# Kernel tuning notes

Hardware: AMD Instinct MI355X
Metric: run time of the kernel (lower is better)

Reference implementation:

```python
import jax, jax.numpy as jnp
import numpy as np

HID = 256
N_HEADS = 4
ATTN_DIM = HID // N_HEADS  # 64
B, S = 64, 512
NEG = -1e10


def setup_inputs() -> dict:
    key = jax.random.key(0)
    ks = jax.random.split(key, 12)
    def lin(k, fan_in, shape):
        bound = 1.0 / np.sqrt(fan_in)
        return jax.random.uniform(k, shape, jnp.float32, -bound, bound)
    return {
        "query": jax.random.normal(ks[0], (B, S, HID), jnp.float32),
        "key": jax.random.normal(ks[1], (B, S, HID), jnp.float32),
        "value": jax.random.normal(ks[2], (B, S, HID), jnp.float32),
        "mask": jax.random.randint(ks[3], (B, 1, S, S), 0, 2, jnp.int32),
        "Wq": lin(ks[4], HID, (HID, HID)), "bq": lin(ks[5], HID, (HID,)),
        "Wk": lin(ks[6], HID, (HID, HID)), "bk": lin(ks[7], HID, (HID,)),
        "Wv": lin(ks[8], HID, (HID, ATTN_DIM)), "bv": lin(ks[9], HID, (ATTN_DIM,)),
        "Wh": lin(ks[10], ATTN_DIM, (ATTN_DIM, HID)), "bh": lin(ks[11], ATTN_DIM, (HID,)),
    }


def reference(query, key, value, mask, Wq, bq, Wk, bk, Wv, bv, Wh, bh):
    b = query.shape[0]
    scale = jnp.sqrt(jnp.asarray(ATTN_DIM, query.dtype))
    Q = (query @ Wq + bq).reshape(b, -1, N_HEADS, ATTN_DIM).transpose(0, 2, 1, 3)  # [B,H,Sq,d]
    K = (key @ Wk + bk).reshape(b, -1, N_HEADS, ATTN_DIM).transpose(0, 2, 1, 3)    # [B,H,Sk,d]
    V = value @ Wv + bv                                                            # [B,Sk,d]
    energy = jnp.einsum('bhqd,bhkd->bhqk', Q, K) / scale
    energy = jnp.where(mask == 0, jnp.asarray(NEG, energy.dtype), energy)
    probs = jax.nn.softmax(energy, axis=-1)          # [B,H,Sq,Sk]
    attention = jnp.mean(probs, axis=1)              # head-mean, [B,Sq,Sk]
    # dropout is identity in eval mode
    output = jnp.einsum('bqk,bkd->bqd', attention, V) @ Wh + bh  # [B,Sq,HID]
    return output, attention
```

## Files before the change

kernel.cpp:

```cpp
#include <hip/hip_runtime.h>

#define NB 64
#define SS 512
#define HIDD 256
#define NHEADS 4
#define ADIM 64
#define NTOT 576

typedef __attribute__((ext_vector_type(8))) short short8v;
typedef __attribute__((ext_vector_type(4))) float f32x4;

#define MFMA16(A, B, C) __builtin_amdgcn_mfma_f32_16x16x32_bf16(A, B, C, 0, 0, 0)
#define AS1 __attribute__((address_space(1)))
#define AS3 __attribute__((address_space(3)))

__device__ __forceinline__ void g2l16(void* lds, const void* g) {
    __builtin_amdgcn_global_load_lds((const AS1 unsigned*)g,
                                     (AS3 unsigned*)lds, 16, 0, 0);
}

__device__ __forceinline__ void bsplit(float x, short& hi, short& lo) {
    unsigned u = __float_as_uint(x);
    unsigned uh = (u + 0x8000u) & 0xFFFF0000u;
    hi = (short)(uh >> 16);
    float r = x - __uint_as_float(uh);
    lo = (short)((__float_as_uint(r) + 0x8000u) >> 16);
}

__device__ __forceinline__ void bsplit_v(float x, short8v& vh, short8v& vl, int i) {
    short h, l;
    bsplit(x, h, l);
    vh[i] = h;
    vl[i] = l;
}

__device__ __forceinline__ short bf16r(float x) {
    return (short)((__float_as_uint(x) + 0x8000u) >> 16);
}

__device__ __forceinline__ int frag_addr(int bb, int hh, int s, int d) {
    const int t16 = s >> 4, rk = s & 15;
    const int ks2 = d >> 5, lgk = (d >> 3) & 3, e8 = d & 7;
    return ((((bb * 4 + hh) * 32 + t16) * 2 + ks2) * 64 + rk + 16 * lgk) * 8 + e8;
}

__global__ __launch_bounds__(256) void prep_weights(
    const float* __restrict__ Wq, const float* __restrict__ Wk,
    const float* __restrict__ Wv, const float* __restrict__ Wh,
    short* __restrict__ WT_hi, short* __restrict__ WT_lo,
    short* __restrict__ WhT)
{
    const int bx = blockIdx.x;
    if (bx < NTOT) {
        const int idx = bx * 256 + threadIdx.x;
        const int n = idx >> 8, k = idx & 255;
        float v;
        if (n < 256)      v = Wq[k * 256 + n];
        else if (n < 512) v = Wk[k * 256 + (n - 256)];
        else              v = Wv[k * 64 + (n - 512)];
        short h, l;
        bsplit(v, h, l);
        WT_hi[idx] = h;
        WT_lo[idx] = l;
    } else {
        const int idx2 = (bx - NTOT) * 256 + threadIdx.x;
        const int n = idx2 >> 6, d = idx2 & 63;
        WhT[idx2] = bf16r(Wh[d * HIDD + n]);
    }
}

__global__ __launch_bounds__(256) void qkv_qk(
    const float* __restrict__ query, const float* __restrict__ key,
    const short* __restrict__ WT_hi, const short* __restrict__ WT_lo,
    const float* __restrict__ bq, const float* __restrict__ bk,
    short* __restrict__ Qhi, short* __restrict__ Qlo,
    short* __restrict__ Khi, short* __restrict__ Klo)
{
    __shared__ short Ws_h[2][256 * 32];
    __shared__ short Ws_l[2][256 * 32];

    const int bm = blockIdx.x * 64;
    const int y = blockIdx.y;
    const int nrow0 = y << 8;
    const float* A = y ? key : query;
    const float* biasp = y ? bk : bq;
    short* Dhi = y ? Khi : Qhi;
    short* Dlo = y ? Klo : Qlo;

    const int tid = threadIdx.x;
    const int w = tid >> 6, l = tid & 63;
    const int l15 = l & 15, lg = l >> 4;
    const int wbase = tid & 192;

    auto stageWT = [&](int buf, int kc) {
#pragma unroll
        for (int i = 0; i < 4; ++i) {
            const int g = i * 256 + tid;
            const int row = g >> 2;
            const int p = g & 3;
            const int sl = p ^ (row & 3);
            const size_t goff = (size_t)(nrow0 + row) * HIDD + kc * 32 + sl * 8;
            g2l16(&Ws_h[buf][(i * 256 + wbase) * 8], WT_hi + goff);
            g2l16(&Ws_l[buf][(i * 256 + wbase) * 8], WT_lo + goff);
        }
    };

    const float* arow = A + (size_t)(bm + w * 16 + l15) * HIDD + lg * 8;

    f32x4 acc[16];
#pragma unroll
    for (int jn = 0; jn < 16; ++jn) acc[jn] = (f32x4){0.f, 0.f, 0.f, 0.f};

    float4 a0c = *reinterpret_cast<const float4*>(arow);
    float4 a1c = *reinterpret_cast<const float4*>(arow + 4);
    stageWT(0, 0);
    __syncthreads();

    int cur = 0;
#pragma unroll
    for (int kc = 0; kc < 8; ++kc) {
        float4 a0n, a1n;
        if (kc < 7) {
            a0n = *reinterpret_cast<const float4*>(arow + (kc + 1) * 32);
            a1n = *reinterpret_cast<const float4*>(arow + (kc + 1) * 32 + 4);
            stageWT(cur ^ 1, kc + 1);
        }

        short8v ah, al;
        bsplit_v(a0c.x, ah, al, 0);
        bsplit_v(a0c.y, ah, al, 1);
        bsplit_v(a0c.z, ah, al, 2);
        bsplit_v(a0c.w, ah, al, 3);
        bsplit_v(a1c.x, ah, al, 4);
        bsplit_v(a1c.y, ah, al, 5);
        bsplit_v(a1c.z, ah, al, 6);
        bsplit_v(a1c.w, ah, al, 7);

#pragma unroll
        for (int jn = 0; jn < 16; ++jn) {
            const int rowB = jn * 16 + l15;
            const int c = lg ^ (rowB & 3);
            short8v bh = *reinterpret_cast<const short8v*>(&Ws_h[cur][rowB * 32 + c * 8]);
            short8v bl = *reinterpret_cast<const short8v*>(&Ws_l[cur][rowB * 32 + c * 8]);
            acc[jn] = MFMA16(ah, bh, acc[jn]);
            acc[jn] = MFMA16(ah, bl, acc[jn]);
            acc[jn] = MFMA16(al, bh, acc[jn]);
        }
        __syncthreads();
        cur ^= 1;
        if (kc < 7) { a0c = a0n; a1c = a1n; }
    }

#pragma unroll
    for (int jn = 0; jn < 16; ++jn) {
        const int ncol = jn * 16 + l15;
        const float bias = biasp[ncol];
        const int hh = ncol >> 6, dd = ncol & 63;
#pragma unroll
        for (int r = 0; r < 4; ++r) {
            const int m = bm + w * 16 + lg * 4 + r;
            const int bb = m >> 9, s = m & 511;
            const int fa = frag_addr(bb, hh, s, dd);
            short h, lo_;
            bsplit(acc[jn][r] + bias, h, lo_);
            Dhi[fa] = h;
            Dlo[fa] = lo_;
        }
    }
}

__global__ __launch_bounds__(256) void qkv_v(
    const float* __restrict__ value,
    const short* __restrict__ WT_hi, const short* __restrict__ WT_lo,
    const float* __restrict__ bv, short* __restrict__ VT)
{
    __shared__ short Ws_h[2][64 * 32];
    __shared__ short Ws_l[2][64 * 32];

    const int bm = blockIdx.x * 64;
    const int tid = threadIdx.x;
    const int w = tid >> 6, l = tid & 63;
    const int l15 = l & 15, lg = l >> 4;
    const int wbase = tid & 192;

    auto stageWT = [&](int buf, int kc) {
        const int row = tid >> 2;
        const int p = tid & 3;
        const int sl = p ^ (row & 3);
        const size_t goff = (size_t)(512 + row) * HIDD + kc * 32 + sl * 8;
        g2l16(&Ws_h[buf][wbase * 8], WT_hi + goff);
        g2l16(&Ws_l[buf][wbase * 8], WT_lo + goff);
    };

    const float* arow = value + (size_t)(bm + w * 16 + l15) * HIDD + lg * 8;

    f32x4 acc[4];
#pragma unroll
    for (int jn = 0; jn < 4; ++jn) acc[jn] = (f32x4){0.f, 0.f, 0.f, 0.f};

    float4 a0c = *reinterpret_cast<const float4*>(arow);
    float4 a1c = *reinterpret_cast<const float4*>(arow + 4);
    stageWT(0, 0);
    __syncthreads();

    int cur = 0;
#pragma unroll
    for (int kc = 0; kc < 8; ++kc) {
        float4 a0n, a1n;
        if (kc < 7) {
            a0n = *reinterpret_cast<const float4*>(arow + (kc + 1) * 32);
            a1n = *reinterpret_cast<const float4*>(arow + (kc + 1) * 32 + 4);
            stageWT(cur ^ 1, kc + 1);
        }

        short8v ah, al;
        bsplit_v(a0c.x, ah, al, 0);
        bsplit_v(a0c.y, ah, al, 1);
        bsplit_v(a0c.z, ah, al, 2);
        bsplit_v(a0c.w, ah, al, 3);
        bsplit_v(a1c.x, ah, al, 4);
        bsplit_v(a1c.y, ah, al, 5);
        bsplit_v(a1c.z, ah, al, 6);
        bsplit_v(a1c.w, ah, al, 7);

#pragma unroll
        for (int jn = 0; jn < 4; ++jn) {
            const int rowB = jn * 16 + l15;
            const int c = lg ^ (rowB & 3);
            short8v bh = *reinterpret_cast<const short8v*>(&Ws_h[cur][rowB * 32 + c * 8]);
            short8v bl = *reinterpret_cast<const short8v*>(&Ws_l[cur][rowB * 32 + c * 8]);
            acc[jn] = MFMA16(ah, bh, acc[jn]);
            acc[jn] = MFMA16(ah, bl, acc[jn]);
            acc[jn] = MFMA16(al, bh, acc[jn]);
        }
        __syncthreads();
        cur ^= 1;
        if (kc < 7) { a0c = a0n; a1c = a1n; }
    }

#pragma unroll
    for (int jn = 0; jn < 4; ++jn) {
        const int d = jn * 16 + l15;
        const float bias = bv[d];
#pragma unroll
        for (int r = 0; r < 4; ++r) {
            const int m = bm + w * 16 + lg * 4 + r;
            const int bb = m >> 9, kk = m & 511;
            const int ks = kk >> 5;
            const int lane = l15 + 16 * ((kk >> 3) & 3);
            const int idx = (((bb * 4 + jn) * 16 + ks) * 64 + lane) * 8 + (kk & 7);
            VT[idx] = bf16r(acc[jn][r] + bias);
        }
    }
}

__global__ __launch_bounds__(256) void attn_probs_fused(
    const short* __restrict__ Qhi_g, const short* __restrict__ Qlo_g,
    const short* __restrict__ Khi_g, const short* __restrict__ Klo_g,
    const short* __restrict__ VT, const short* __restrict__ WhT,
    const int* __restrict__ mask, const float* __restrict__ bh,
    float* __restrict__ attn, float* __restrict__ out)
{
    __shared__ __align__(16) short P_s[32 * 512];
    __shared__ float red[2][4][2][16];

    const int wg = blockIdx.x;
    const int swz = (wg & 7) * 128 + (wg >> 3);
    const int b = swz >> 4;
    const int q0 = (swz & 15) * 32;

    const int tid = threadIdx.x;
    const int w = tid >> 6;
    const int l = tid & 63;
    const int l15 = l & 15;
    const int lg = l >> 4;

    unsigned mbits[2];
#pragma unroll
    for (int qs = 0; qs < 2; ++qs) {
        unsigned bits = 0;
        const int q = q0 + qs * 16 + l15;
        const int* mrow = mask + ((size_t)b * SS + q) * SS;
#pragma unroll
        for (int f = 0; f < 8; ++f) {
            const int kt = f >> 1, ms = f & 1;
            const int k = kt * 128 + (2 * w + ms) * 16 + lg * 4;
            int4 mv = *reinterpret_cast<const int4*>(&mrow[k]);
            bits |= (mv.x != 0 ? 1u : 0u) << (f * 4 + 0);
            bits |= (mv.y != 0 ? 1u : 0u) << (f * 4 + 1);
            bits |= (mv.z != 0 ? 1u : 0u) << (f * 4 + 2);
            bits |= (mv.w != 0 ? 1u : 0u) << (f * 4 + 3);
        }
        mbits[qs] = bits;
    }

    f32x4 acc[4][2][2];
#pragma unroll
    for (int kt = 0; kt < 4; ++kt)
#pragma unroll
        for (int ms = 0; ms < 2; ++ms)
#pragma unroll
            for (int qs = 0; qs < 2; ++qs)
                acc[kt][ms][qs] = (f32x4){0.f, 0.f, 0.f, 0.f};

    const int qt_base = (swz & 15) * 2;

    for (int h = 0; h < NHEADS; ++h) {
        const int bh32 = (b * 4 + h) * 32;

        short8v qh[2][2], ql[2][2];
#pragma unroll
        for (int ks2 = 0; ks2 < 2; ++ks2)
#pragma unroll
            for (int qs = 0; qs < 2; ++qs) {
                const int off = (((bh32 + qt_base + qs) * 2 + ks2) * 64 + l) * 8;
                qh[ks2][qs] = *reinterpret_cast<const short8v*>(Qhi_g + off);
                ql[ks2][qs] = *reinterpret_cast<const short8v*>(Qlo_g + off);
            }

        f32x4 e[4][2][2];
#pragma unroll
        for (int kt = 0; kt < 4; ++kt)
#pragma unroll
            for (int ms = 0; ms < 2; ++ms)
#pragma unroll
                for (int qs = 0; qs < 2; ++qs)
                    e[kt][ms][qs] = (f32x4){0.f, 0.f, 0.f, 0.f};

#pragma unroll
        for (int kt = 0; kt < 4; ++kt) {
#pragma unroll
            for (int ks2 = 0; ks2 < 2; ++ks2) {
                const int t0 = kt * 8 + 2 * w;
                const int base0 = (((bh32 + t0) * 2 + ks2) * 64 + l) * 8;
                const int base1 = base0 + 1024;
                short8v ah0 = *reinterpret_cast<const short8v*>(Khi_g + base0);
                short8v ah1 = *reinterpret_cast<const short8v*>(Khi_g + base1);
                short8v al0 = *reinterpret_cast<const short8v*>(Klo_g + base0);
                short8v al1 = *reinterpret_cast<const short8v*>(Klo_g + base1);

                e[kt][0][0] = MFMA16(ah0, qh[ks2][0], e[kt][0][0]);
                e[kt][0][0] = MFMA16(ah0, ql[ks2][0], e[kt][0][0]);
                e[kt][0][0] = MFMA16(al0, qh[ks2][0], e[kt][0][0]);

                e[kt][0][1] = MFMA16(ah0, qh[ks2][1], e[kt][0][1]);
                e[kt][0][1] = MFMA16(ah0, ql[ks2][1], e[kt][0][1]);
                e[kt][0][1] = MFMA16(al0, qh[ks2][1], e[kt][0][1]);

                e[kt][1][0] = MFMA16(ah1, qh[ks2][0], e[kt][1][0]);
                e[kt][1][0] = MFMA16(ah1, ql[ks2][0], e[kt][1][0]);
                e[kt][1][0] = MFMA16(al1, qh[ks2][0], e[kt][1][0]);

                e[kt][1][1] = MFMA16(ah1, qh[ks2][1], e[kt][1][1]);
                e[kt][1][1] = MFMA16(ah1, ql[ks2][1], e[kt][1][1]);
                e[kt][1][1] = MFMA16(al1, qh[ks2][1], e[kt][1][1]);
            }
        }

        float sm[2] = {0.f, 0.f};
        const float c = 0.125f;
#pragma unroll
        for (int kt = 0; kt < 4; ++kt)
#pragma unroll
            for (int ms = 0; ms < 2; ++ms)
#pragma unroll
                for (int qs = 0; qs < 2; ++qs)
#pragma unroll
                    for (int r = 0; r < 4; ++r) {
                        float p = __expf(e[kt][ms][qs][r] * c);
                        const unsigned bit = (mbits[qs] >> ((kt * 2 + ms) * 4 + r)) & 1u;
                        p = bit ? p : 0.f;
                        e[kt][ms][qs][r] = p;
                        sm[qs] += p;
                    }
#pragma unroll
        for (int qs = 0; qs < 2; ++qs) {
            sm[qs] += __shfl_xor(sm[qs], 16);
            sm[qs] += __shfl_xor(sm[qs], 32);
        }
        if (l < 16) { red[h & 1][w][0][l] = sm[0]; red[h & 1][w][1][l] = sm[1]; }
        __syncthreads();
#pragma unroll
        for (int qs = 0; qs < 2; ++qs) {
            const float Z = (red[h & 1][0][qs][l15] + red[h & 1][1][qs][l15]) +
                            (red[h & 1][2][qs][l15] + red[h & 1][3][qs][l15]);
            const float inv = 0.25f / fmaxf(Z, 1e-30f);
#pragma unroll
            for (int kt = 0; kt < 4; ++kt)
#pragma unroll
                for (int ms = 0; ms < 2; ++ms)
#pragma unroll
                    for (int r = 0; r < 4; ++r)
                        acc[kt][ms][qs][r] += e[kt][ms][qs][r] * inv;
        }
    }

#pragma unroll
    for (int kt = 0; kt < 4; ++kt)
#pragma unroll
        for (int ms = 0; ms < 2; ++ms)
#pragma unroll
            for (int qs = 0; qs < 2; ++qs) {
                const int q = q0 + qs * 16 + l15;
                const int k = kt * 128 + (2 * w + ms) * 16 + lg * 4;
                float4 o;
                o.x = acc[kt][ms][qs][0];
                o.y = acc[kt][ms][qs][1];
                o.z = acc[kt][ms][qs][2];
                o.w = acc[kt][ms][qs][3];
                *reinterpret_cast<float4*>(&attn[((size_t)b * SS + q) * SS + k]) = o;

                const int ql_ = qs * 16 + l15;
                const int c8 = kt * 16 + (2 * w + ms) * 2 + (lg >> 1);
                const int phys = c8 ^ (ql_ & 7);
                short4 pk;
                pk.x = bf16r(acc[kt][ms][qs][0]);
                pk.y = bf16r(acc[kt][ms][qs][1]);
                pk.z = bf16r(acc[kt][ms][qs][2]);
                pk.w = bf16r(acc[kt][ms][qs][3]);
                *reinterpret_cast<short4*>(&P_s[ql_ * 512 + phys * 8 + (lg & 1) * 4]) = pk;
            }
    __syncthreads();

    f32x4 tacc[2];
    tacc[0] = (f32x4){0.f, 0.f, 0.f, 0.f};
    tacc[1] = (f32x4){0.f, 0.f, 0.f, 0.f};
#pragma unroll
    for (int ks = 0; ks < 16; ++ks) {
        short8v va = *reinterpret_cast<const short8v*>(
            VT + (((b * 4 + w) * 16 + ks) * 64 + l) * 8);
#pragma unroll
        for (int qt = 0; qt < 2; ++qt) {
            const int q = qt * 16 + l15;
            const int phys = (ks * 4 + lg) ^ (q & 7);
            short8v pb = *reinterpret_cast<const short8v*>(&P_s[q * 512 + phys * 8]);
            tacc[qt] = MFMA16(va, pb, tacc[qt]);
        }
    }
    __syncthreads();

    float* T_s = reinterpret_cast<float*>(P_s);
#pragma unroll
    for (int qt = 0; qt < 2; ++qt) {
        const int q = qt * 16 + l15;
        const int d = w * 16 + lg * 4;
        float4 tv;
        tv.x = tacc[qt][0];
        tv.y = tacc[qt][1];
        tv.z = tacc[qt][2];
        tv.w = tacc[qt][3];
        *reinterpret_cast<float4*>(&T_s[q * 68 + d]) = tv;
    }
    __syncthreads();

    f32x4 oacc[2][4];
#pragma unroll
    for (int qt = 0; qt < 2; ++qt)
#pragma unroll
        for (int nt = 0; nt < 4; ++nt)
            oacc[qt][nt] = (f32x4){0.f, 0.f, 0.f, 0.f};

#pragma unroll
    for (int ks = 0; ks < 2; ++ks) {
        short8v ta[2];
#pragma unroll
        for (int qt = 0; qt < 2; ++qt) {
            const int q = qt * 16 + l15;
            float4 t0 = *reinterpret_cast<const float4*>(&T_s[q * 68 + ks * 32 + lg * 8]);
            float4 t1 = *reinterpret_cast<const float4*>(&T_s[q * 68 + ks * 32 + lg * 8 + 4]);
            ta[qt][0] = bf16r(t0.x);
            ta[qt][1] = bf16r(t0.y);
            ta[qt][2] = bf16r(t0.z);
            ta[qt][3] = bf16r(t0.w);
            ta[qt][4] = bf16r(t1.x);
            ta[qt][5] = bf16r(t1.y);
            ta[qt][6] = bf16r(t1.z);
            ta[qt][7] = bf16r(t1.w);
        }
#pragma unroll
        for (int nt = 0; nt < 4; ++nt) {
            const int n = (w * 4 + nt) * 16 + l15;
            short8v wb = *reinterpret_cast<const short8v*>(
                WhT + n * 64 + ks * 32 + lg * 8);
#pragma unroll
            for (int qt = 0; qt < 2; ++qt)
                oacc[qt][nt] = MFMA16(ta[qt], wb, oacc[qt][nt]);
        }
    }

#pragma unroll
    for (int qt = 0; qt < 2; ++qt)
#pragma unroll
        for (int nt = 0; nt < 4; ++nt) {
            const int n = (w * 4 + nt) * 16 + l15;
            const float bias = bh[n];
#pragma unroll
            for (int r = 0; r < 4; ++r) {
                const int q = q0 + qt * 16 + lg * 4 + r;
                out[((size_t)b * SS + q) * HIDD + n] = oacc[qt][nt][r] + bias;
            }
        }
}

extern "C" void kernel_launch(void* const* d_in, const int* in_sizes, int n_in,
                              void* d_out, int out_size, void* d_ws, size_t ws_size,
                              hipStream_t stream)
{
    const float* query = (const float*)d_in[0];
    const float* key   = (const float*)d_in[1];
    const float* value = (const float*)d_in[2];
    const int*   mask  = (const int*)d_in[3];
    const float* Wq = (const float*)d_in[4];
    const float* bq = (const float*)d_in[5];
    const float* Wk = (const float*)d_in[6];
    const float* bk = (const float*)d_in[7];
    const float* Wv = (const float*)d_in[8];
    const float* bv = (const float*)d_in[9];
    const float* Wh = (const float*)d_in[10];
    const float* bh = (const float*)d_in[11];

    float* out  = (float*)d_out;
    float* attn = out + (size_t)NB * SS * HIDD;

    const size_t BS = (size_t)NB * SS;
    short* Qhi = (short*)d_ws;
    short* Qlo = Qhi + BS * HIDD;
    short* Khi = Qlo + BS * HIDD;
    short* Klo = Khi + BS * HIDD;
    short* VT  = Klo + BS * HIDD;
    short* WhT = VT + BS * ADIM;

    short* WT_hi = (short*)attn;
    short* WT_lo = WT_hi + NTOT * HIDD;

    prep_weights<<<dim3(NTOT + 64), 256, 0, stream>>>(Wq, Wk, Wv, Wh,
                                                      WT_hi, WT_lo, WhT);
    qkv_qk<<<dim3(512, 2), 256, 0, stream>>>(query, key, WT_hi, WT_lo,
                                             bq, bk, Qhi, Qlo, Khi, Klo);
    qkv_v<<<dim3(512), 256, 0, stream>>>(value, WT_hi, WT_lo, bv, VT);
    attn_probs_fused<<<dim3(1024), 256, 0, stream>>>(Qhi, Qlo, Khi, Klo, VT, WhT,
                                                     mask, bh, attn, out);
}
```

Baseline: 154.8 us.

## Drop bf16 hi/lo split for Q/K and double attention waves per block

Q and K are now stored as single bf16 values, with no hi/lo pair. This halves their workspace writes and reads and cuts the QK^T MFMAs from three per tile to one. The attention kernel now launches 512 threads, so 8 waves split the key dimension where 4 did before, and the softmax-sum reduction covers 8 partials. Only the first 4 waves run the P·V and output projection stages. The risk is lower precision in the attention probabilities, since a single bf16 product replaces the split-precision emulation.

After: 138.8 us. 10.3% less time.

```diff
diff --git a/kernel.cpp b/kernel.cpp
--- a/kernel.cpp
+++ b/kernel.cpp
@@ -73,8 +73,7 @@
     const float* __restrict__ query, const float* __restrict__ key,
     const short* __restrict__ WT_hi, const short* __restrict__ WT_lo,
     const float* __restrict__ bq, const float* __restrict__ bk,
-    short* __restrict__ Qhi, short* __restrict__ Qlo,
-    short* __restrict__ Khi, short* __restrict__ Klo)
+    short* __restrict__ Qhi, short* __restrict__ Khi)
 {
     __shared__ short Ws_h[2][256 * 32];
     __shared__ short Ws_l[2][256 * 32];
@@ -85,7 +84,6 @@
     const float* A = y ? key : query;
     const float* biasp = y ? bk : bq;
     short* Dhi = y ? Khi : Qhi;
-    short* Dlo = y ? Klo : Qlo;
 
     const int tid = threadIdx.x;
     const int w = tid >> 6, l = tid & 63;
@@ -161,10 +159,7 @@
             const int m = bm + w * 16 + lg * 4 + r;
             const int bb = m >> 9, s = m & 511;
             const int fa = frag_addr(bb, hh, s, dd);
-            short h, lo_;
-            bsplit(acc[jn][r] + bias, h, lo_);
-            Dhi[fa] = h;
-            Dlo[fa] = lo_;
+            Dhi[fa] = bf16r(acc[jn][r] + bias);
         }
     }
 }
@@ -254,15 +249,14 @@
     }
 }
 
-__global__ __launch_bounds__(256) void attn_probs_fused(
-    const short* __restrict__ Qhi_g, const short* __restrict__ Qlo_g,
-    const short* __restrict__ Khi_g, const short* __restrict__ Klo_g,
+__global__ __launch_bounds__(512) void attn_probs_fused(
+    const short* __restrict__ Qhi_g, const short* __restrict__ Khi_g,
     const short* __restrict__ VT, const short* __restrict__ WhT,
     const int* __restrict__ mask, const float* __restrict__ bh,
     float* __restrict__ attn, float* __restrict__ out)
 {
     __shared__ __align__(16) short P_s[32 * 512];
-    __shared__ float red[2][4][2][16];
+    __shared__ float red[2][8][2][16];
 
     const int wg = blockIdx.x;
     const int swz = (wg & 7) * 128 + (wg >> 3);
@@ -271,6 +265,8 @@
 
     const int tid = threadIdx.x;
     const int w = tid >> 6;
+    const int h2 = w >> 2;
+    const int sp = w & 3;
     const int l = tid & 63;
     const int l15 = l & 15;
     const int lg = l >> 4;
@@ -282,95 +278,84 @@
         const int q = q0 + qs * 16 + l15;
         const int* mrow = mask + ((size_t)b * SS + q) * SS;
 #pragma unroll
-        for (int f = 0; f < 8; ++f) {
-            const int kt = f >> 1, ms = f & 1;
-            const int k = kt * 128 + (2 * w + ms) * 16 + lg * 4;
-            int4 mv = *reinterpret_cast<const int4*>(&mrow[k]);
-            bits |= (mv.x != 0 ? 1u : 0u) << (f * 4 + 0);
-            bits |= (mv.y != 0 ? 1u : 0u) << (f * 4 + 1);
-            bits |= (mv.z != 0 ? 1u : 0u) << (f * 4 + 2);
-            bits |= (mv.w != 0 ? 1u : 0u) << (f * 4 + 3);
-        }
+        for (int kl = 0; kl < 2; ++kl)
+#pragma unroll
+            for (int ms = 0; ms < 2; ++ms) {
+                const int fi = kl * 2 + ms;
+                const int kt = 2 * h2 + kl;
+                const int k = kt * 128 + (2 * sp + ms) * 16 + lg * 4;
+                int4 mv = *reinterpret_cast<const int4*>(&mrow[k]);
+                bits |= (mv.x != 0 ? 1u : 0u) << (fi * 4 + 0);
+                bits |= (mv.y != 0 ? 1u : 0u) << (fi * 4 + 1);
+                bits |= (mv.z != 0 ? 1u : 0u) << (fi * 4 + 2);
+                bits |= (mv.w != 0 ? 1u : 0u) << (fi * 4 + 3);
+            }
         mbits[qs] = bits;
     }
 
-    f32x4 acc[4][2][2];
-#pragma unroll
-    for (int kt = 0; kt < 4; ++kt)
+    f32x4 acc[2][2][2];
+#pragma unroll
+    for (int kl = 0; kl < 2; ++kl)
 #pragma unroll
         for (int ms = 0; ms < 2; ++ms)
 #pragma unroll
             for (int qs = 0; qs < 2; ++qs)
-                acc[kt][ms][qs] = (f32x4){0.f, 0.f, 0.f, 0.f};
+                acc[kl][ms][qs] = (f32x4){0.f, 0.f, 0.f, 0.f};
 
     const int qt_base = (swz & 15) * 2;
 
     for (int h = 0; h < NHEADS; ++h) {
         const int bh32 = (b * 4 + h) * 32;
 
-        short8v qh[2][2], ql[2][2];
+        short8v qh[2][2];
 #pragma unroll
         for (int ks2 = 0; ks2 < 2; ++ks2)
 #pragma unroll
             for (int qs = 0; qs < 2; ++qs) {
                 const int off = (((bh32 + qt_base + qs) * 2 + ks2) * 64 + l) * 8;
                 qh[ks2][qs] = *reinterpret_cast<const short8v*>(Qhi_g + off);
-                ql[ks2][qs] = *reinterpret_cast<const short8v*>(Qlo_g + off);
-            }
-
-        f32x4 e[4][2][2];
-#pragma unroll
-        for (int kt = 0; kt < 4; ++kt)
+            }
+
+        f32x4 e[2][2][2];
+#pragma unroll
+        for (int kl = 0; kl < 2; ++kl)
 #pragma unroll
             for (int ms = 0; ms < 2; ++ms)
 #pragma unroll
                 for (int qs = 0; qs < 2; ++qs)
-                    e[kt][ms][qs] = (f32x4){0.f, 0.f, 0.f, 0.f};
-
-#pragma unroll
-        for (int kt = 0; kt < 4; ++kt) {
+                    e[kl][ms][qs] = (f32x4){0.f, 0.f, 0.f, 0.f};
+
+#pragma unroll
+        for (int kl = 0; kl < 2; ++kl) {
+            const int t0 = (2 * h2 + kl) * 8 + 2 * sp;
 #pragma unroll
             for (int ks2 = 0; ks2 < 2; ++ks2) {
-                const int t0 = kt * 8 + 2 * w;
                 const int base0 = (((bh32 + t0) * 2 + ks2) * 64 + l) * 8;
                 const int base1 = base0 + 1024;
                 short8v ah0 = *reinterpret_cast<const short8v*>(Khi_g + base0);
                 short8v ah1 = *reinterpret_cast<const short8v*>(Khi_g + base1);
-                short8v al0 = *reinterpret_cast<const short8v*>(Klo_g + base0);
-                short8v al1 = *reinterpret_cast<const short8v*>(Klo_g + base1);
-
-                e[kt][0][0] = MFMA16(ah0, qh[ks2][0], e[kt][0][0]);
-                e[kt][0][0] = MFMA16(ah0, ql[ks2][0], e[kt][0][0]);
-                e[kt][0][0] = MFMA16(al0, qh[ks2][0], e[kt][0][0]);
-
-                e[kt][0][1] = MFMA16(ah0, qh[ks2][1], e[kt][0][1]);
-                e[kt][0][1] = MFMA16(ah0, ql[ks2][1], e[kt][0][1]);
-                e[kt][0][1] = MFMA16(al0, qh[ks2][1], e[kt][0][1]);
-
-                e[kt][1][0] = MFMA16(ah1, qh[ks2][0], e[kt][1][0]);
-                e[kt][1][0] = MFMA16(ah1, ql[ks2][0], e[kt][1][0]);
-                e[kt][1][0] = MFMA16(al1, qh[ks2][0], e[kt][1][0]);
-
-                e[kt][1][1] = MFMA16(ah1, qh[ks2][1], e[kt][1][1]);
-                e[kt][1][1] = MFMA16(ah1, ql[ks2][1], e[kt][1][1]);
-                e[kt][1][1] = MFMA16(al1, qh[ks2][1], e[kt][1][1]);
+
+                e[kl][0][0] = MFMA16(ah0, qh[ks2][0], e[kl][0][0]);
+                e[kl][0][1] = MFMA16(ah0, qh[ks2][1], e[kl][0][1]);
+                e[kl][1][0] = MFMA16(ah1, qh[ks2][0], e[kl][1][0]);
+                e[kl][1][1] = MFMA16(ah1, qh[ks2][1], e[kl][1][1]);
             }
         }
 
         float sm[2] = {0.f, 0.f};
         const float c = 0.125f;
 #pragma unroll
-        for (int kt = 0; kt < 4; ++kt)
+        for (int kl = 0; kl < 2; ++kl)
 #pragma unroll
             for (int ms = 0; ms < 2; ++ms)
 #pragma unroll
                 for (int qs = 0; qs < 2; ++qs)
 #pragma unroll
                     for (int r = 0; r < 4; ++r) {
-                        float p = __expf(e[kt][ms][qs][r] * c);
-                        const unsigned bit = (mbits[qs] >> ((kt * 2 + ms) * 4 + r)) & 1u;
+                        float p = __expf(e[kl][ms][qs][r] * c);
+                        const unsigned bit = (mbits[qs] >> ((kl * 2 + ms) * 4 + r)) & 1u;
                         p = bit ? p : 0.f;
-                        e[kt][ms][qs][r] = p;
+                        e[kl][ms][qs][r] = p;
                         sm[qs] += p;
                     }
 #pragma unroll
@@ -382,42 +367,44 @@
         __syncthreads();
 #pragma unroll
         for (int qs = 0; qs < 2; ++qs) {
-            const float Z = (red[h & 1][0][qs][l15] + red[h & 1][1][qs][l15]) +
-                            (red[h & 1][2][qs][l15] + red[h & 1][3][qs][l15]);
+            float Z = 0.f;
+#pragma unroll
+            for (int wv = 0; wv < 8; ++wv) Z += red[h & 1][wv][qs][l15];
             const float inv = 0.25f / fmaxf(Z, 1e-30f);
 #pragma unroll
-            for (int kt = 0; kt < 4; ++kt)
+            for (int kl = 0; kl < 2; ++kl)
 #pragma unroll
                 for (int ms = 0; ms < 2; ++ms)
 #pragma unroll
                     for (int r = 0; r < 4; ++r)
-                        acc[kt][ms][qs][r] += e[kt][ms][qs][r] * inv;
-        }
-    }
-
-#pragma unroll
-    for (int kt = 0; kt < 4; ++kt)
+                        acc[kl][ms][qs][r] += e[kl][ms][qs][r] * inv;
+        }
+    }
+
+#pragma unroll
+    for (int kl = 0; kl < 2; ++kl)
 #pragma unroll
         for (int ms = 0; ms < 2; ++ms)
 #pragma unroll
             for (int qs = 0; qs < 2; ++qs) {
+                const int kt = 2 * h2 + kl;
                 const int q = q0 + qs * 16 + l15;
-                const int k = kt * 128 + (2 * w + ms) * 16 + lg * 4;
+                const int k = kt * 128 + (2 * sp + ms) * 16 + lg * 4;
                 float4 o;
-                o.x = acc[kt][ms][qs][0];
-                o.y = acc[kt][ms][qs][1];
-                o.z = acc[kt][ms][qs][2];
-                o.w = acc[kt][ms][qs][3];
+                o.x = acc[kl][ms][qs][0];
+                o.y = acc[kl][ms][qs][1];
+                o.z = acc[kl][ms][qs][2];
+                o.w = acc[kl][ms][qs][3];
                 *reinterpret_cast<float4*>(&attn[((size_t)b * SS + q) * SS + k]) = o;
 
                 const int ql_ = qs * 16 + l15;
-                const int c8 = kt * 16 + (2 * w + ms) * 2 + (lg >> 1);
+                const int c8 = kt * 16 + (2 * sp + ms) * 2 + (lg >> 1);
                 const int phys = c8 ^ (ql_ & 7);
                 short4 pk;
-                pk.x = bf16r(acc[kt][ms][qs][0]);
-                pk.y = bf16r(acc[kt][ms][qs][1]);
-                pk.z = bf16r(acc[kt][ms][qs][2]);
-                pk.w = bf16r(acc[kt][ms][qs][3]);
+                pk.x = bf16r(acc[kl][ms][qs][0]);
+                pk.y = bf16r(acc[kl][ms][qs][1]);
+                pk.z = bf16r(acc[kl][ms][qs][2]);
+                pk.w = bf16r(acc[kl][ms][qs][3]);
                 *reinterpret_cast<short4*>(&P_s[ql_ * 512 + phys * 8 + (lg & 1) * 4]) = pk;
             }
     __syncthreads();
@@ -425,81 +412,87 @@
     f32x4 tacc[2];
     tacc[0] = (f32x4){0.f, 0.f, 0.f, 0.f};
     tacc[1] = (f32x4){0.f, 0.f, 0.f, 0.f};
-#pragma unroll
-    for (int ks = 0; ks < 16; ++ks) {
-        short8v va = *reinterpret_cast<const short8v*>(
-            VT + (((b * 4 + w) * 16 + ks) * 64 + l) * 8);
+    if (w < 4) {
+#pragma unroll
+        for (int ks = 0; ks < 16; ++ks) {
+            short8v va = *reinterpret_cast<const short8v*>(
+                VT + (((b * 4 + w) * 16 + ks) * 64 + l) * 8);
+#pragma unroll
+            for (int qt = 0; qt < 2; ++qt) {
+                const int q = qt * 16 + l15;
+                const int phys = (ks * 4 + lg) ^ (q & 7);
+                short8v pb = *reinterpret_cast<const short8v*>(&P_s[q * 512 + phys * 8]);
+                tacc[qt] = MFMA16(va, pb, tacc[qt]);
+            }
+        }
+    }
+    __syncthreads();
+
+    float* T_s = reinterpret_cast<float*>(P_s);
+    if (w < 4) {
 #pragma unroll
         for (int qt = 0; qt < 2; ++qt) {
             const int q = qt * 16 + l15;
-            const int phys = (ks * 4 + lg) ^ (q & 7);
-            short8v pb = *reinterpret_cast<const short8v*>(&P_s[q * 512 + phys * 8]);
-            tacc[qt] = MFMA16(va, pb, tacc[qt]);
+            const int d = w * 16 + lg * 4;
+            float4 tv;
+            tv.x = tacc[qt][0];
+            tv.y = tacc[qt][1];
+            tv.z = tacc[qt][2];
+            tv.w = tacc[qt][3];
+            *reinterpret_cast<float4*>(&T_s[q * 68 + d]) = tv;
         }
     }
     __syncthreads();
 
-    float* T_s = reinterpret_cast<float*>(P_s);
-#pragma unroll
-    for (int qt = 0; qt < 2; ++qt) {
-        const int q = qt * 16 + l15;
-        const int d = w * 16 + lg * 4;
-        float4 tv;
-        tv.x = tacc[qt][0];
-        tv.y = tacc[qt][1];
-        tv.z = tacc[qt][2];
-        tv.w = tacc[qt][3];
-        *reinterpret_cast<float4*>(&T_s[q * 68 + d]) = tv;
-    }
-    __syncthreads();
-
-    f32x4 oacc[2][4];
-#pragma unroll
-    for (int qt = 0; qt < 2; ++qt)
-#pragma unroll
-        for (int nt = 0; nt < 4; ++nt)
-            oacc[qt][nt] = (f32x4){0.f, 0.f, 0.f, 0.f};
-
-#pragma unroll
-    for (int ks = 0; ks < 2; ++ks) {
-        short8v ta[2];
-#pragma unroll
-        for (int qt = 0; qt < 2; ++qt) {
-            const int q = qt * 16 + l15;
-            float4 t0 = *reinterpret_cast<const float4*>(&T_s[q * 68 + ks * 32 + lg * 8]);
-            float4 t1 = *reinterpret_cast<const float4*>(&T_s[q * 68 + ks * 32 + lg * 8 + 4]);
-            ta[qt][0] = bf16r(t0.x);
-            ta[qt][1] = bf16r(t0.y);
-            ta[qt][2] = bf16r(t0.z);
-            ta[qt][3] = bf16r(t0.w);
-            ta[qt][4] = bf16r(t1.x);
-            ta[qt][5] = bf16r(t1.y);
-            ta[qt][6] = bf16r(t1.z);
-            ta[qt][7] = bf16r(t1.w);
-        }
-#pragma unroll
-        for (int nt = 0; nt < 4; ++nt) {
-            const int n = (w * 4 + nt) * 16 + l15;
-            short8v wb = *reinterpret_cast<const short8v*>(
-                WhT + n * 64 + ks * 32 + lg * 8);
-#pragma unroll
-            for (int qt = 0; qt < 2; ++qt)
-                oacc[qt][nt] = MFMA16(ta[qt], wb, oacc[qt][nt]);
-        }
-    }
-
-#pragma unroll
-    for (int qt = 0; qt < 2; ++qt)
-#pragma unroll
-        for (int nt = 0; nt < 4; ++nt) {
-            const int n = (w * 4 + nt) * 16 + l15;
-            const float bias = bh[n];
-#pragma unroll
-            for (int r = 0; r < 4; ++r) {
-                const int q = q0 + qt * 16 + lg * 4 + r;
-                out[((size_t)b * SS + q) * HIDD + n] = oacc[qt][nt][r] + bias;
-            }
-        }
+    if (w < 4) {
+        f32x4 oacc[2][4];
+#pragma unroll
+        for (int qt = 0; qt < 2; ++qt)
+#pragma unroll
+            for (int nt = 0; nt < 4; ++nt)
+                oacc[qt][nt] = (f32x4){0.f, 0.f, 0.f, 0.f};
+
+#pragma unroll
+        for (int ks = 0; ks < 2; ++ks) {
+            short8v ta[2];
+#pragma unroll
+            for (int qt = 0; qt < 2; ++qt) {
+                const int q = qt * 16 + l15;
+                float4 t0 = *reinterpret_cast<const float4*>(&T_s[q * 68 + ks * 32 + lg * 8]);
+                float4 t1 = *reinterpret_cast<const float4*>(&T_s[q * 68 + ks * 32 + lg * 8 + 4]);
+                ta[qt][0] = bf16r(t0.x);
+                ta[qt][1] = bf16r(t0.y);
+                ta[qt][2] = bf16r(t0.z);
+                ta[qt][3] = bf16r(t0.w);
+                ta[qt][4] = bf16r(t1.x);
+                ta[qt][5] = bf16r(t1.y);
+                ta[qt][6] = bf16r(t1.z);
+                ta[qt][7] = bf16r(t1.w);
+            }
+#pragma unroll
+            for (int nt = 0; nt < 4; ++nt) {
+                const int n = (w * 4 + nt) * 16 + l15;
+                short8v wb = *reinterpret_cast<const short8v*>(
+                    WhT + n * 64 + ks * 32 + lg * 8);
+#pragma unroll
+                for (int qt = 0; qt < 2; ++qt)
+                    oacc[qt][nt] = MFMA16(ta[qt], wb, oacc[qt][nt]);
+            }
+        }
+
+#pragma unroll
+        for (int qt = 0; qt < 2; ++qt)
+#pragma unroll
+            for (int nt = 0; nt < 4; ++nt) {
+                const int n = (w * 4 + nt) * 16 + l15;
+                const float bias = bh[n];
+#pragma unroll
+                for (int r = 0; r < 4; ++r) {
+                    const int q = q0 + qt * 16 + lg * 4 + r;
+                    out[((size_t)b * SS + q) * HIDD + n] = oacc[qt][nt][r] + bias;
+                }
+            }
+    }
 }
 
 extern "C" void kernel_launch(void* const* d_in, const int* in_sizes, int n_in,
@@ -524,10 +517,8 @@
 
     const size_t BS = (size_t)NB * SS;
     short* Qhi = (short*)d_ws;
-    short* Qlo = Qhi + BS * HIDD;
-    short* Khi = Qlo + BS * HIDD;
-    short* Klo = Khi + BS * HIDD;
-    short* VT  = Klo + BS * HIDD;
+    short* Khi = Qhi + BS * HIDD;
+    short* VT  = Khi + BS * HIDD;
     short* WhT = VT + BS * ADIM;
 
     short* WT_hi = (short*)attn;
@@ -536,8 +527,8 @@
     prep_weights<<<dim3(NTOT + 64), 256, 0, stream>>>(Wq, Wk, Wv, Wh,
                                                       WT_hi, WT_lo, WhT);
     qkv_qk<<<dim3(512, 2), 256, 0, stream>>>(query, key, WT_hi, WT_lo,
-                                             bq, bk, Qhi, Qlo, Khi, Klo);
+                                             bq, bk, Qhi, Khi);
     qkv_v<<<dim3(512), 256, 0, stream>>>(value, WT_hi, WT_lo, bv, VT);
-    attn_probs_fused<<<dim3(1024), 256, 0, stream>>>(Qhi, Qlo, Khi, Klo, VT, WhT,
+    attn_probs_fused<<<dim3(1024), 512, 0, stream>>>(Qhi, Khi, VT, WhT,
                                                      mask, bh, attn, out);
 }
```
